# Kernel optimization log

Measured on AMD Instinct MI355X. Metric: run time of the kernel, lower is better.

The kernel has to match this reference:

```python
import jax, jax.numpy as jnp
import numpy as np

RESOLUTION = 2048
NUM_BEAMS = 256
K0 = 50.0
TWO_PI = 2.0 * np.pi


def setup_inputs() -> dict:
    key = jax.random.key(0)
    ks = jax.random.split(key, 6)
    # meshgrid buffers (indexing='ij')
    x = jnp.linspace(-1.0, 1.0, RESOLUTION, dtype=jnp.float32)
    y = jnp.linspace(-1.0, 1.0, RESOLUTION, dtype=jnp.float32)
    X, Y = jnp.meshgrid(x, y, indexing='ij')
    return {
        'theta': jax.random.uniform(ks[0], (NUM_BEAMS,), jnp.float32) * TWO_PI,
        'real': jax.random.normal(ks[1], (NUM_BEAMS,), jnp.float32) * 0.1,
        'imag': jax.random.normal(ks[2], (NUM_BEAMS,), jnp.float32) * 0.1,
        'x0': jax.random.uniform(ks[3], (NUM_BEAMS,), jnp.float32) * 2.0 - 1.0,
        'y0': jax.random.uniform(ks[4], (NUM_BEAMS,), jnp.float32) * 2.0 - 1.0,
        'log_sigma': jnp.zeros((NUM_BEAMS,), jnp.float32),
        'X': X,
        'Y': Y,
    }


def reference(theta, real, imag, x0, y0, log_sigma, X, Y):
    # Accumulate E = sum_i coeff_i * exp(i*phase_i) * envelope_i over beams,
    # carrying (E_re, E_im) through a scan so only grid-sized buffers live at once.
    def body(carry, p):
        E_re, E_im = carry
        th, re, im, px, py, ls = p
        kx = K0 * jnp.cos(th)
        ky = K0 * jnp.sin(th)
        sigma = jnp.exp(ls) + 0.001
        env = jnp.exp(-((X - px) ** 2 + (Y - py) ** 2) / sigma ** 2)
        phase = kx * X + ky * Y
        c = jnp.cos(phase)
        s = jnp.sin(phase)
        # (re + i*im) * (c + i*s) * env
        E_re = E_re + env * (re * c - im * s)
        E_im = E_im + env * (re * s + im * c)
        return (E_re, E_im), None

    params = jnp.stack([theta, real, imag, x0, y0, log_sigma], axis=1)  # [B, 6]
    zero = jnp.zeros_like(X)
    (E_re, E_im), _ = jax.lax.scan(body, (zero, zero), params)
    return E_re ** 2 + E_im ** 2  # |E|^2
```

## Files before the change

kernel.cpp:

```cpp
#include <hip/hip_runtime.h>
#include <math.h>

#define RES 2048
#define NB  256

typedef _Float16 f16;
typedef _Float16 f16x8 __attribute__((ext_vector_type(8)));
typedef float    f32x16 __attribute__((ext_vector_type(16)));

#define BM 128
#define BN 128
#define BK 16
#define NKT (NB / BK)
#define PL  (BM * BK)

__device__ __forceinline__ f16x8 neg8(f16x8 v) {
    union { f16x8 h; unsigned int u[4]; } x;
    x.h = v;
    #pragma unroll
    for (int i = 0; i < 4; ++i) x.u[i] ^= 0x80008000u;
    return x.h;
}

__global__ __launch_bounds__(512) void ewald_fused(
    const float* __restrict__ theta, const float* __restrict__ reA,
    const float* __restrict__ imA, const float* __restrict__ x0A,
    const float* __restrict__ y0A, const float* __restrict__ lsA,
    const float* __restrict__ X, const float* __restrict__ Y,
    float* __restrict__ out)
{
    __shared__ f16 smA[2][2][BM][BK];
    __shared__ f16 smB[2][2][BN][BK];
    __shared__ float skx[NB], sky[NB], sre[NB], sim[NB],
                     spx[NB], spy[NB], sis2[NB];
    __shared__ float sX[BM], sY[BN];

    const int t    = threadIdx.x;
    const int lane = t & 63;
    const int wave = t >> 6;
    const int wm   = wave >> 2;
    const int wn   = wave & 3;
    const int la   = lane & 31;
    const int lg   = lane >> 5;

    const int flat = blockIdx.x;
    const int swz  = (flat & 7) * 32 + (flat >> 3);
    const int m0   = (swz >> 4) * BM;
    const int n0   = (swz & 15) * BN;

    if (t < 128) {
        sX[t] = X[(size_t)(m0 + t) * RES];
    } else if (t < 256) {
        sY[t - 128] = Y[n0 + (t - 128)];
    } else {
        const int b = t - 256;
        float s, c;
        __sincosf(theta[b], &s, &c);
        skx[b] = 50.0f * c;
        sky[b] = 50.0f * s;
        const float sig = __expf(lsA[b]) + 0.001f;
        sis2[b] = 1.0f / (sig * sig);
        sre[b] = reA[b]; sim[b] = imA[b];
        spx[b] = x0A[b]; spy[b] = y0A[b];
    }
    __syncthreads();

    const int kk2 = (t & 7) * 2;
    const int grp = t >> 3;

    #define EVAL(bf, kt)                                                      \
    do {                                                                      \
        const int b0_ = (kt) * BK + kk2;                                      \
        float aR_[2][2], aI_[2][2], bR_[2][2], bI_[2][2];                     \
        _Pragma("unroll")                                                     \
        for (int jb = 0; jb < 2; ++jb) {                                      \
            const int b_ = b0_ + jb;                                          \
            const float kx = skx[b_], ky = sky[b_];                           \
            const float re = sre[b_], im = sim[b_];                           \
            const float px = spx[b_], py = spy[b_];                           \
            const float is2 = sis2[b_];                                       \
            _Pragma("unroll")                                                 \
            for (int r = 0; r < 2; ++r) {                                     \
                const int row = grp * 2 + r;                                  \
                float s_, c_;                                                 \
                const float xv = sX[row];                                     \
                __sincosf(kx * xv, &s_, &c_);                                 \
                const float dx = xv - px;                                     \
                const float ex = __expf(-dx * dx * is2);                      \
                aR_[jb][r] = ex * (re * c_ - im * s_);                        \
                aI_[jb][r] = ex * (re * s_ + im * c_);                        \
                const float yv = sY[row];                                     \
                __sincosf(ky * yv, &s_, &c_);                                 \
                const float dy = yv - py;                                     \
                const float ey = __expf(-dy * dy * is2);                      \
                bR_[jb][r] = ey * c_;                                         \
                bI_[jb][r] = ey * s_;                                         \
            }                                                                 \
        }                                                                     \
        _Pragma("unroll")                                                     \
        for (int r = 0; r < 2; ++r) {                                         \
            const int row = grp * 2 + r;                                      \
            union { f16 h[2]; unsigned int u; } p_;                           \
            p_.h[0] = (f16)aR_[0][r]; p_.h[1] = (f16)aR_[1][r];               \
            *(unsigned int*)&smA[bf][0][row][kk2] = p_.u;                     \
            p_.h[0] = (f16)aI_[0][r]; p_.h[1] = (f16)aI_[1][r];               \
            *(unsigned int*)&smA[bf][1][row][kk2] = p_.u;                     \
            p_.h[0] = (f16)bR_[0][r]; p_.h[1] = (f16)bR_[1][r];               \
            *(unsigned int*)&smB[bf][0][row][kk2] = p_.u;                     \
            p_.h[0] = (f16)bI_[0][r]; p_.h[1] = (f16)bI_[1][r];               \
            *(unsigned int*)&smB[bf][1][row][kk2] = p_.u;                     \
        }                                                                     \
    } while (0)

    const int offA0 = (wm * 64 +  0 + la) * BK + lg * 8;
    const int offA1 = (wm * 64 + 32 + la) * BK + lg * 8;
    const int offB  = (wn * 32 + la) * BK + lg * 8;

    f32x16 accRe0 = (f32x16)0.0f, accIm0 = (f32x16)0.0f;
    f32x16 accRe1 = (f32x16)0.0f, accIm1 = (f32x16)0.0f;

    EVAL(0, 0);
    __syncthreads();

    for (int kt = 0; kt < NKT; ++kt) {
        const f16* sA = &smA[kt & 1][0][0][0];
        const f16* sB = &smB[kt & 1][0][0][0];
        const f16x8 aR0 = *(const f16x8*)(sA + offA0);
        const f16x8 aR1 = *(const f16x8*)(sA + offA1);
        const f16x8 aI0 = *(const f16x8*)(sA + PL + offA0);
        const f16x8 aI1 = *(const f16x8*)(sA + PL + offA1);
        const f16x8 bR  = *(const f16x8*)(sB + offB);
        const f16x8 bI  = *(const f16x8*)(sB + PL + offB);
        const f16x8 bN  = neg8(bI);

        accRe0 = __builtin_amdgcn_mfma_f32_32x32x16_f16(aR0, bR, accRe0, 0, 0, 0);
        accIm0 = __builtin_amdgcn_mfma_f32_32x32x16_f16(aR0, bI, accIm0, 0, 0, 0);
        accRe1 = __builtin_amdgcn_mfma_f32_32x32x16_f16(aR1, bR, accRe1, 0, 0, 0);
        accIm1 = __builtin_amdgcn_mfma_f32_32x32x16_f16(aR1, bI, accIm1, 0, 0, 0);
        accRe0 = __builtin_amdgcn_mfma_f32_32x32x16_f16(aI0, bN, accRe0, 0, 0, 0);
        accIm0 = __builtin_amdgcn_mfma_f32_32x32x16_f16(aI0, bR, accIm0, 0, 0, 0);
        accRe1 = __builtin_amdgcn_mfma_f32_32x32x16_f16(aI1, bN, accRe1, 0, 0, 0);
        accIm1 = __builtin_amdgcn_mfma_f32_32x32x16_f16(aI1, bR, accIm1, 0, 0, 0);

        if (kt + 1 < NKT)
            EVAL((kt + 1) & 1, kt + 1);

        __syncthreads();
    }

    const int gn     = n0 + wn * 32 + la;
    const int gmBase = m0 + wm * 64;
    #pragma unroll
    for (int r = 0; r < 16; ++r) {
        const int row = (r & 3) + 8 * (r >> 2) + 4 * lg;
        const float er = accRe0[r], ei = accIm0[r];
        out[(size_t)(gmBase + row) * RES + gn] = er * er + ei * ei;
    }
    #pragma unroll
    for (int r = 0; r < 16; ++r) {
        const int row = (r & 3) + 8 * (r >> 2) + 4 * lg;
        const float er = accRe1[r], ei = accIm1[r];
        out[(size_t)(gmBase + 32 + row) * RES + gn] = er * er + ei * ei;
    }
    #undef EVAL
}

extern "C" void kernel_launch(void* const* d_in, const int* in_sizes, int n_in,
                              void* d_out, int out_size, void* d_ws, size_t ws_size,
                              hipStream_t stream) {
    const float* theta = (const float*)d_in[0];
    const float* reA   = (const float*)d_in[1];
    const float* imA   = (const float*)d_in[2];
    const float* x0A   = (const float*)d_in[3];
    const float* y0A   = (const float*)d_in[4];
    const float* lsA   = (const float*)d_in[5];
    const float* X     = (const float*)d_in[6];
    const float* Y     = (const float*)d_in[7];
    float* out = (float*)d_out;

    ewald_fused<<<256, 512, 0, stream>>>(theta, reA, imA, x0A, y0A, lsA,
                                         X, Y, out);
}
```

Baseline: 24.58 us.

## Swizzle LDS tiles, pack beam params as float4, and reorder eval before MFMAs

The A/B fragment tiles in shared memory now use an XOR-swizzled index so the 16-byte fragment reads and the 4-byte writes spread across LDS banks instead of conflicting. Per-beam parameters are packed into two float4 arrays, so each beam needs two vector LDS loads instead of seven scalar ones. The next tile's trig/exp evaluation is now issued before the MFMA block, and the MFMAs are wrapped in s_setprio, so VALU work can overlap with matrix work across waves. The swizzle adds some index arithmetic, and the changed instruction order depends on the compiler and scheduler to produce real overlap.

```diff
diff --git a/kernel.cpp b/kernel.cpp
--- a/kernel.cpp
+++ b/kernel.cpp
@@ -22,6 +22,10 @@
     return x.h;
 }
 
+__device__ __forceinline__ int swzE(int row, int k) {
+    return (row * BK + k) ^ ((row & 7) << 3);
+}
+
 __global__ __launch_bounds__(512) void ewald_fused(
     const float* __restrict__ theta, const float* __restrict__ reA,
     const float* __restrict__ imA, const float* __restrict__ x0A,
@@ -29,10 +33,10 @@
     const float* __restrict__ X, const float* __restrict__ Y,
     float* __restrict__ out)
 {
-    __shared__ f16 smA[2][2][BM][BK];
-    __shared__ f16 smB[2][2][BN][BK];
-    __shared__ float skx[NB], sky[NB], sre[NB], sim[NB],
-                     spx[NB], spy[NB], sis2[NB];
+    __shared__ f16 smA[2][2][PL];
+    __shared__ f16 smB[2][2][PL];
+    __shared__ float4 sP0[NB];
+    __shared__ float4 sP1[NB];
     __shared__ float sX[BM], sY[BN];
 
     const int t    = threadIdx.x;
@@ -56,12 +60,9 @@
         const int b = t - 256;
         float s, c;
         __sincosf(theta[b], &s, &c);
-        skx[b] = 50.0f * c;
-        sky[b] = 50.0f * s;
         const float sig = __expf(lsA[b]) + 0.001f;
-        sis2[b] = 1.0f / (sig * sig);
-        sre[b] = reA[b]; sim[b] = imA[b];
-        spx[b] = x0A[b]; spy[b] = y0A[b];
+        sP0[b] = make_float4(50.0f * c, 50.0f * s, x0A[b], y0A[b]);
+        sP1[b] = make_float4(reA[b], imA[b], 1.0f / (sig * sig), 0.0f);
     }
     __syncthreads();
 
@@ -74,25 +75,22 @@
         float aR_[2][2], aI_[2][2], bR_[2][2], bI_[2][2];                     \
         _Pragma("unroll")                                                     \
         for (int jb = 0; jb < 2; ++jb) {                                      \
-            const int b_ = b0_ + jb;                                          \
-            const float kx = skx[b_], ky = sky[b_];                           \
-            const float re = sre[b_], im = sim[b_];                           \
-            const float px = spx[b_], py = spy[b_];                           \
-            const float is2 = sis2[b_];                                       \
+            const float4 p0 = sP0[b0_ + jb];                                  \
+            const float4 p1 = sP1[b0_ + jb];                                  \
             _Pragma("unroll")                                                 \
             for (int r = 0; r < 2; ++r) {                                     \
                 const int row = grp * 2 + r;                                  \
                 float s_, c_;                                                 \
                 const float xv = sX[row];                                     \
-                __sincosf(kx * xv, &s_, &c_);                                 \
-                const float dx = xv - px;                                     \
-                const float ex = __expf(-dx * dx * is2);                      \
-                aR_[jb][r] = ex * (re * c_ - im * s_);                        \
-                aI_[jb][r] = ex * (re * s_ + im * c_);                        \
+                __sincosf(p0.x * xv, &s_, &c_);                               \
+                const float dx = xv - p0.z;                                   \
+                const float ex = __expf(-dx * dx * p1.z);                     \
+                aR_[jb][r] = ex * (p1.x * c_ - p1.y * s_);                    \
+                aI_[jb][r] = ex * (p1.x * s_ + p1.y * c_);                    \
                 const float yv = sY[row];                                     \
-                __sincosf(ky * yv, &s_, &c_);                                 \
-                const float dy = yv - py;                                     \
-                const float ey = __expf(-dy * dy * is2);                      \
+                __sincosf(p0.y * yv, &s_, &c_);                               \
+                const float dy = yv - p0.w;                                   \
+                const float ey = __expf(-dy * dy * p1.z);                     \
                 bR_[jb][r] = ey * c_;                                         \
                 bI_[jb][r] = ey * s_;                                         \
             }                                                                 \
@@ -100,21 +98,22 @@
         _Pragma("unroll")                                                     \
         for (int r = 0; r < 2; ++r) {                                         \
             const int row = grp * 2 + r;                                      \
+            const int e_ = swzE(row, kk2);                                    \
             union { f16 h[2]; unsigned int u; } p_;                           \
             p_.h[0] = (f16)aR_[0][r]; p_.h[1] = (f16)aR_[1][r];               \
-            *(unsigned int*)&smA[bf][0][row][kk2] = p_.u;                     \
+            *(unsigned int*)&smA[bf][0][e_] = p_.u;                           \
             p_.h[0] = (f16)aI_[0][r]; p_.h[1] = (f16)aI_[1][r];               \
-            *(unsigned int*)&smA[bf][1][row][kk2] = p_.u;                     \
+            *(unsigned int*)&smA[bf][1][e_] = p_.u;                           \
             p_.h[0] = (f16)bR_[0][r]; p_.h[1] = (f16)bR_[1][r];               \
-            *(unsigned int*)&smB[bf][0][row][kk2] = p_.u;                     \
+            *(unsigned int*)&smB[bf][0][e_] = p_.u;                           \
             p_.h[0] = (f16)bI_[0][r]; p_.h[1] = (f16)bI_[1][r];               \
-            *(unsigned int*)&smB[bf][1][row][kk2] = p_.u;                     \
+            *(unsigned int*)&smB[bf][1][e_] = p_.u;                           \
         }                                                                     \
     } while (0)
 
-    const int offA0 = (wm * 64 +  0 + la) * BK + lg * 8;
-    const int offA1 = (wm * 64 + 32 + la) * BK + lg * 8;
-    const int offB  = (wn * 32 + la) * BK + lg * 8;
+    const int offA0 = swzE(wm * 64 +  0 + la, lg * 8);
+    const int offA1 = swzE(wm * 64 + 32 + la, lg * 8);
+    const int offB  = swzE(wn * 32 + la, lg * 8);
 
     f32x16 accRe0 = (f32x16)0.0f, accIm0 = (f32x16)0.0f;
     f32x16 accRe1 = (f32x16)0.0f, accIm1 = (f32x16)0.0f;
@@ -123,16 +122,19 @@
     __syncthreads();
 
     for (int kt = 0; kt < NKT; ++kt) {
-        const f16* sA = &smA[kt & 1][0][0][0];
-        const f16* sB = &smB[kt & 1][0][0][0];
-        const f16x8 aR0 = *(const f16x8*)(sA + offA0);
-        const f16x8 aR1 = *(const f16x8*)(sA + offA1);
-        const f16x8 aI0 = *(const f16x8*)(sA + PL + offA0);
-        const f16x8 aI1 = *(const f16x8*)(sA + PL + offA1);
-        const f16x8 bR  = *(const f16x8*)(sB + offB);
-        const f16x8 bI  = *(const f16x8*)(sB + PL + offB);
+        const int cur = kt & 1;
+        const f16x8 aR0 = *(const f16x8*)&smA[cur][0][offA0];
+        const f16x8 aR1 = *(const f16x8*)&smA[cur][0][offA1];
+        const f16x8 aI0 = *(const f16x8*)&smA[cur][1][offA0];
+        const f16x8 aI1 = *(const f16x8*)&smA[cur][1][offA1];
+        const f16x8 bR  = *(const f16x8*)&smB[cur][0][offB];
+        const f16x8 bI  = *(const f16x8*)&smB[cur][1][offB];
         const f16x8 bN  = neg8(bI);
 
+        if (kt + 1 < NKT)
+            EVAL(cur ^ 1, kt + 1);
+
+        __builtin_amdgcn_s_setprio(1);
         accRe0 = __builtin_amdgcn_mfma_f32_32x32x16_f16(aR0, bR, accRe0, 0, 0, 0);
         accIm0 = __builtin_amdgcn_mfma_f32_32x32x16_f16(aR0, bI, accIm0, 0, 0, 0);
         accRe1 = __builtin_amdgcn_mfma_f32_32x32x16_f16(aR1, bR, accRe1, 0, 0, 0);
@@ -141,9 +143,7 @@
         accIm0 = __builtin_amdgcn_mfma_f32_32x32x16_f16(aI0, bR, accIm0, 0, 0, 0);
         accRe1 = __builtin_amdgcn_mfma_f32_32x32x16_f16(aI1, bN, accRe1, 0, 0, 0);
         accIm1 = __builtin_amdgcn_mfma_f32_32x32x16_f16(aI1, bR, accIm1, 0, 0, 0);
-
-        if (kt + 1 < NKT)
-            EVAL((kt + 1) & 1, kt + 1);
+        __builtin_amdgcn_s_setprio(0);
 
         __syncthreads();
     }
```

Measured after the change: 25.10 us. 1.02x slower.
